# Kernel optimization log

Measured on AMD Instinct MI355X. Metric: run time of the kernel, lower is better.

## Reference

```python
import jax, jax.numpy as jnp
import numpy as np

H, D, K = 8, 512, 64
EPS = 1e-12


def _l2norm(x):
    # F.normalize(p=2, dim=-1): x / max(||x||_2, eps)
    n = jnp.sqrt(jnp.sum(x * x, axis=-1, keepdims=True))
    return x / jnp.maximum(n, EPS)


def setup_inputs() -> dict:
    key = jax.random.key(0)
    ks = jax.random.split(key, 8)
    S, B = 1024, 16
    scale = 1.0 / np.sqrt(D)
    return {
        "query": jax.random.normal(ks[0], (S, B, D), dtype=jnp.float32),
        "key": jax.random.normal(ks[1], (S, B, D), dtype=jnp.float32),
        "value": jax.random.normal(ks[2], (S, B, D), dtype=jnp.float32),
        # stacked per-head projection weights, torch Linear convention [out,in]
        "WQ": jax.random.uniform(ks[3], (H, K, D), jnp.float32, -scale, scale),
        "WK": jax.random.uniform(ks[4], (H, K, D), jnp.float32, -scale, scale),
        "WV": jax.random.uniform(ks[5], (H, K, D), jnp.float32, -scale, scale),
        "Wout": jax.random.uniform(ks[6], (D, H * K), jnp.float32,
                                   -1.0 / np.sqrt(H * K), 1.0 / np.sqrt(H * K)),
    }


def reference(query, key, value, WQ, WK, WV, Wout):
    temp = K ** 0.5
    # project all heads at once: [S,B,D] x [H,K,D] -> [B,H,S,K]
    wq = _l2norm(jnp.einsum("sbd,hkd->bhsk", query, WQ))
    wk = _l2norm(jnp.einsum("sbd,hkd->bhsk", key, WK))
    wv = _l2norm(jnp.einsum("sbd,hkd->bhsk", value, WV))
    # cosine-similarity attention scores [B,H,Sq,Sk]
    scores = jnp.einsum("bhsk,bhtk->bhst", wq, wk) / temp
    aff = jax.nn.softmax(scores, axis=-1)
    out = jnp.einsum("bhst,bhtk->bhsk", aff, wv)  # [B,H,S,K]
    # concat heads -> [S,B,H*K] (matches torch per-head concat on last dim)
    Sq, B = query.shape[0], query.shape[1]
    concat = out.transpose(2, 0, 1, 3).reshape(Sq, B, H * K)
    return concat @ Wout.T  # [S,B,D]
```

## Files before the change

kernel.cpp:

```cpp
#include <hip/hip_runtime.h>
#include <cstdint>
#include <cstddef>

typedef unsigned int u32;
typedef unsigned short u16;
typedef __attribute__((ext_vector_type(8))) short short8;
typedef __attribute__((ext_vector_type(4))) float f32x4;

#define S_LEN 1024
#define BATCH 16
#define NHEAD 8
#define DMODEL 512
#define KHD 64
#define NROW (S_LEN * BATCH)

__device__ __forceinline__ u16 f2bf(float f) {
    u32 u = __float_as_uint(f);
    return (u16)((u + 0x7fffu + ((u >> 16) & 1u)) >> 16);
}

__device__ __forceinline__ void gl_lds16(const void* g, void* l) {
    __builtin_amdgcn_global_load_lds(
        (const __attribute__((address_space(1))) void*)(uintptr_t)g,
        (__attribute__((address_space(3))) void*)(uintptr_t)l, 16, 0, 0);
}

__global__ __launch_bounds__(256) void wcvt_kernel(
    const float* __restrict__ WQ, const float* __restrict__ WK,
    const float* __restrict__ WV, const float* __restrict__ Wo,
    u16* __restrict__ dst)
{
    const int m = blockIdx.y;
    const float* __restrict__ src = (m == 0) ? WQ : (m == 1) ? WK : (m == 2) ? WV : Wo;
    const int idx = (blockIdx.x * 256 + threadIdx.x) * 4;
    const float4 v = *(const float4*)(src + idx);
    u16 r[4];
    r[0] = f2bf(v.x); r[1] = f2bf(v.y); r[2] = f2bf(v.z); r[3] = f2bf(v.w);
    *(uint2*)(dst + (size_t)m * DMODEL * DMODEL + idx) = *(uint2*)r;
}

__global__ __launch_bounds__(256) void xcvt_kernel(
    const float* __restrict__ s0, const float* __restrict__ s1,
    u16* __restrict__ dst)
{
    const float* __restrict__ src = (blockIdx.y == 0) ? s0 : s1;
    u16* d = dst + (size_t)blockIdx.y * NROW * DMODEL;
    const int idx = (blockIdx.x * 256 + threadIdx.x) * 4;
    const float4 v = *(const float4*)(src + idx);
    u16 r[4];
    r[0] = f2bf(v.x); r[1] = f2bf(v.y); r[2] = f2bf(v.z); r[3] = f2bf(v.w);
    *(uint2*)(d + idx) = *(uint2*)r;
}

template<int M>
__global__ __launch_bounds__(256) void gemm_kernel(
    const u16* __restrict__ Abf,
    const u16* __restrict__ Wb,
    u16* __restrict__ outN,
    float* __restrict__ outP)
{
    __shared__ __align__(16) u16 Alds[128 * 64];
    __shared__ __align__(16) u16 Blds[128 * 64];

    const int tid  = threadIdx.x;
    const int wave = tid >> 6;
    const int lane = tid & 63;
    const int m16  = lane & 15;
    const int quad = lane >> 4;
    const int wm   = wave >> 1;
    const int wn   = wave & 1;
    const int n0   = blockIdx.y * 128;
    const int row0 = blockIdx.x * 128;
    const int z    = (M == 1) ? blockIdx.z : 0;
    const int bb   = (M == 2) ? blockIdx.z : 0;

    const u16* __restrict__ A = Abf + (size_t)z * NROW * DMODEL + (size_t)bb * DMODEL;
    const size_t astr = (M == 2) ? (size_t)BATCH * DMODEL : (size_t)DMODEL;
    const u16* __restrict__ B = Wb + ((M == 1) ? (size_t)z * DMODEL * DMODEL : 0);

    f32x4 acc[4][4] = {};

    const int brow   = lane >> 3;
    const int bchunk = (lane & 7) ^ brow;

    for (int kt = 0; kt < DMODEL; kt += 64) {
        __syncthreads();
        {
            const u16* ap = A + (size_t)(row0 + wave * 32 + brow) * astr + kt + bchunk * 8;
            const u16* bp = B + (size_t)(n0 + wave * 32 + brow) * DMODEL + kt + bchunk * 8;
            u16* la = &Alds[(wave * 32) * 64];
            u16* lb = &Blds[(wave * 32) * 64];
#pragma unroll
            for (int j = 0; j < 4; j++) {
                gl_lds16(ap + (size_t)j * 8 * astr,   la + j * 8 * 64);
                gl_lds16(bp + (size_t)j * 8 * DMODEL, lb + j * 8 * 64);
            }
        }
        __syncthreads();

#pragma unroll
        for (int half = 0; half < 2; half++) {
            short8 af[4], bfr[4];
#pragma unroll
            for (int mt = 0; mt < 4; mt++)
                af[mt] = *(const short8*)&Alds[(wm * 64 + mt * 16 + m16) * 64 +
                                               (((half << 2) + quad) ^ (m16 & 7)) * 8];
#pragma unroll
            for (int nt = 0; nt < 4; nt++)
                bfr[nt] = *(const short8*)&Blds[(wn * 64 + nt * 16 + m16) * 64 +
                                                (((half << 2) + quad) ^ (m16 & 7)) * 8];
#pragma unroll
            for (int mt = 0; mt < 4; mt++)
#pragma unroll
                for (int nt = 0; nt < 4; nt++)
                    acc[mt][nt] = __builtin_amdgcn_mfma_f32_16x16x32_bf16(af[mt], bfr[nt], acc[mt][nt], 0, 0, 0);
        }
    }

    if (M == 1) {
        const int h = (n0 >> 6) + wn;
        u16* outZ = outN + (size_t)z * BATCH * NHEAD * S_LEN * KHD;
#pragma unroll
        for (int mt = 0; mt < 4; mt++) {
#pragma unroll
            for (int r = 0; r < 4; r++) {
                float ss = 0.0f;
#pragma unroll
                for (int nt = 0; nt < 4; nt++) ss += acc[mt][nt][r] * acc[mt][nt][r];
                ss += __shfl_xor(ss, 1);
                ss += __shfl_xor(ss, 2);
                ss += __shfl_xor(ss, 4);
                ss += __shfl_xor(ss, 8);
                const float sc = 1.0f / fmaxf(sqrtf(ss), 1e-12f);
                const int i = row0 + wm * 64 + mt * 16 + quad * 4 + r;
                const int s = i >> 4, b = i & 15;
                u16* op = outZ + (((size_t)b * NHEAD + h) * S_LEN + s) * KHD;
#pragma unroll
                for (int nt = 0; nt < 4; nt++)
                    op[nt * 16 + m16] = f2bf(acc[mt][nt][r] * sc);
            }
        }
    } else if (M == 2) {
        const int h = (n0 >> 6) + wn;
#pragma unroll
        for (int mt = 0; mt < 4; mt++) {
            float scl[4];
#pragma unroll
            for (int r = 0; r < 4; r++) {
                float ss = 0.0f;
#pragma unroll
                for (int nt = 0; nt < 4; nt++) ss += acc[mt][nt][r] * acc[mt][nt][r];
                ss += __shfl_xor(ss, 1);
                ss += __shfl_xor(ss, 2);
                ss += __shfl_xor(ss, 4);
                ss += __shfl_xor(ss, 8);
                scl[r] = 1.0f / fmaxf(sqrtf(ss), 1e-12f);
            }
            const int sbase = row0 + wm * 64 + mt * 16 + quad * 4;
#pragma unroll
            for (int nt = 0; nt < 4; nt++) {
                const int vcol = nt * 16 + m16;
                uint2 pk;
                pk.x = (u32)f2bf(acc[mt][nt][0] * scl[0]) |
                       ((u32)f2bf(acc[mt][nt][1] * scl[1]) << 16);
                pk.y = (u32)f2bf(acc[mt][nt][2] * scl[2]) |
                       ((u32)f2bf(acc[mt][nt][3] * scl[3]) << 16);
                u16* dp = outN + (((size_t)bb * NHEAD + h) * KHD + vcol) * S_LEN + sbase;
                *(uint2*)dp = pk;
            }
        }
    } else {
#pragma unroll
        for (int mt = 0; mt < 4; mt++) {
#pragma unroll
            for (int r = 0; r < 4; r++) {
                const int i = row0 + wm * 64 + mt * 16 + quad * 4 + r;
                float* op = outP + (size_t)i * DMODEL + n0 + wn * 64;
#pragma unroll
                for (int nt = 0; nt < 4; nt++)
                    op[nt * 16 + m16] = acc[mt][nt][r];
            }
        }
    }
}

__global__ __launch_bounds__(256, 4) void attn_kernel(
    const u16* __restrict__ wq, const u16* __restrict__ wk, const u16* __restrict__ wvT,
    u16* __restrict__ Xc)
{
    __shared__ __align__(16) u16 Klds[2][64 * 64];
    __shared__ __align__(16) u16 Vlds[2][64 * 64];
    __shared__ __align__(16) u16 Plds[4][2][16 * 32];

    const int tid  = threadIdx.x;
    const int wave = tid >> 6;
    const int lane = tid & 63;
    const int m16  = lane & 15;
    const int quad = lane >> 4;
    const int bh   = blockIdx.x;
    const int qt   = blockIdx.y;

    const u16* Qb = wq  + (size_t)bh * S_LEN * KHD;
    const u16* Kb = wk  + (size_t)bh * S_LEN * KHD;
    const u16* Vb = wvT + (size_t)bh * KHD * S_LEN;

    const int qr0 = qt * 128 + wave * 32 + m16;
    short8 qf[2][2];
    qf[0][0] = *(const short8*)(Qb + (size_t)qr0 * KHD + quad * 8);
    qf[0][1] = *(const short8*)(Qb + (size_t)qr0 * KHD + 32 + quad * 8);
    qf[1][0] = *(const short8*)(Qb + (size_t)(qr0 + 16) * KHD + quad * 8);
    qf[1][1] = *(const short8*)(Qb + (size_t)(qr0 + 16) * KHD + 32 + quad * 8);

    short8 ones;
#pragma unroll
    for (int j = 0; j < 8; j++) ones[j] = (short)0x3F80;

    f32x4 o[2][4] = {};
    f32x4 ls[2]   = {};
    const float C1 = 0.125f, C2 = 0.0078125f;

    const int srow   = lane >> 3;
    const int schunk = (lane & 7) ^ srow;
    const int r0     = wave * 8 + srow;
    const int pswz   = (m16 >> 1) & 3;

    gl_lds16(Kb + (size_t)r0 * KHD + schunk * 8,               &Klds[0][(wave * 8) * 64]);
    gl_lds16(Kb + (size_t)(r0 + 32) * KHD + schunk * 8,        &Klds[0][(wave * 8 + 32) * 64]);
    gl_lds16(Vb + (size_t)r0 * S_LEN + schunk * 8,             &Vlds[0][(wave * 8) * 64]);
    gl_lds16(Vb + (size_t)(r0 + 32) * S_LEN + schunk * 8,      &Vlds[0][(wave * 8 + 32) * 64]);
    __syncthreads();

    for (int it = 0; it < S_LEN / 64; it++) {
        const int cur = it & 1;

        if (it + 1 < S_LEN / 64) {
            const int nxt = cur ^ 1;
            const int kt0 = (it + 1) * 64;
            gl_lds16(Kb + (size_t)(kt0 + r0) * KHD + schunk * 8,        &Klds[nxt][(wave * 8) * 64]);
            gl_lds16(Kb + (size_t)(kt0 + r0 + 32) * KHD + schunk * 8,   &Klds[nxt][(wave * 8 + 32) * 64]);
            gl_lds16(Vb + (size_t)r0 * S_LEN + kt0 + schunk * 8,        &Vlds[nxt][(wave * 8) * 64]);
            gl_lds16(Vb + (size_t)(r0 + 32) * S_LEN + kt0 + schunk * 8, &Vlds[nxt][(wave * 8 + 32) * 64]);
        }

#pragma unroll
        for (int cc = 0; cc < 2; cc++) {
#pragma unroll
            for (int mm = 0; mm < 2; mm++) {
                const int mt = cc * 2 + mm;
                const short8 kf0 = *(const short8*)&Klds[cur][(mt * 16 + m16) * 64 + (quad ^ (m16 & 7)) * 8];
                const short8 kf1 = *(const short8*)&Klds[cur][(mt * 16 + m16) * 64 + ((4 + quad) ^ (m16 & 7)) * 8];
#pragma unroll
                for (int qb = 0; qb < 2; qb++) {
                    f32x4 s = {};
                    s = __builtin_amdgcn_mfma_f32_16x16x32_bf16(kf0, qf[qb][0], s, 0, 0, 0);
                    s = __builtin_amdgcn_mfma_f32_16x16x32_bf16(kf1, qf[qb][1], s, 0, 0, 0);
                    u32 up[4];
#pragma unroll
                    for (int r = 0; r < 4; r++) {
                        const float y = s[r];
                        const float p = fmaf(fmaf(C2, y, C1), y, 1.0f);
                        up[r] = __float_as_uint(p);
                    }
                    uint2 pk;
                    pk.x = __builtin_amdgcn_perm(up[1], up[0], 0x07060302u);
                    pk.y = __builtin_amdgcn_perm(up[3], up[2], 0x07060302u);
                    *(uint2*)((char*)&Plds[wave][qb][0] + m16 * 64 +
                              ((((mm << 1) + (quad >> 1)) ^ pswz) << 4) + ((quad & 1) << 3)) = pk;
                }
            }

            short8 vfr[4];
#pragma unroll
            for (int vt = 0; vt < 4; vt++)
                vfr[vt] = *(const short8*)&Vlds[cur][(vt * 16 + m16) * 64 +
                                                     (((cc << 2) + quad) ^ (m16 & 7)) * 8];
            __builtin_amdgcn_s_setprio(1);
#pragma unroll
            for (int qb = 0; qb < 2; qb++) {
                const short8 pb = *(const short8*)((const char*)&Plds[wave][qb][0] + m16 * 64 +
                                                   ((quad ^ pswz) << 4));
                ls[qb] = __builtin_amdgcn_mfma_f32_16x16x32_bf16(ones, pb, ls[qb], 0, 0, 0);
#pragma unroll
                for (int vt = 0; vt < 4; vt++)
                    o[qb][vt] = __builtin_amdgcn_mfma_f32_16x16x32_bf16(vfr[vt], pb, o[qb][vt], 0, 0, 0);
            }
            __builtin_amdgcn_s_setprio(0);
        }

        __syncthreads();
    }

    const int b = bh >> 3, h = bh & 7;
#pragma unroll
    for (int qb = 0; qb < 2; qb++) {
        const float inv = 1.0f / ls[qb][0];
        const int qrow = qr0 + qb * 16;
        u16* cp = Xc + ((size_t)qrow * BATCH + b) * (NHEAD * KHD) + h * KHD;
#pragma unroll
        for (int vt = 0; vt < 4; vt++) {
            uint2 pk;
            pk.x = (u32)f2bf(o[qb][vt][0] * inv) | ((u32)f2bf(o[qb][vt][1] * inv) << 16);
            pk.y = (u32)f2bf(o[qb][vt][2] * inv) | ((u32)f2bf(o[qb][vt][3] * inv) << 16);
            *(uint2*)(cp + vt * 16 + quad * 4) = pk;
        }
    }
}

extern "C" void kernel_launch(void* const* d_in, const int* in_sizes, int n_in,
                              void* d_out, int out_size, void* d_ws, size_t ws_size,
                              hipStream_t stream) {
    const float* q    = (const float*)d_in[0];
    const float* k    = (const float*)d_in[1];
    const float* v    = (const float*)d_in[2];
    const float* WQ   = (const float*)d_in[3];
    const float* WK   = (const float*)d_in[4];
    const float* WV   = (const float*)d_in[5];
    const float* Wout = (const float*)d_in[6];
    float* out = (float*)d_out;
    u16*  Xbf = (u16*)d_out;

    const size_t per = (size_t)BATCH * NHEAD * S_LEN * KHD;
    u16* wsQKV = (u16*)d_ws;
    u16* wsW   = wsQKV + 3 * per;

    wcvt_kernel<<<dim3(256, 4), 256, 0, stream>>>(WQ, WK, WV, Wout, wsW);

    xcvt_kernel<<<dim3(NROW * DMODEL / 1024, 2), 256, 0, stream>>>(q, k, Xbf);

    gemm_kernel<1><<<dim3(NROW / 128, DMODEL / 128, 2), 256, 0, stream>>>(
        Xbf, wsW, wsQKV, nullptr);

    xcvt_kernel<<<dim3(NROW * DMODEL / 1024, 1), 256, 0, stream>>>(v, v, Xbf);

    gemm_kernel<2><<<dim3(S_LEN / 128, DMODEL / 128, BATCH), 256, 0, stream>>>(
        Xbf, wsW + (size_t)2 * DMODEL * DMODEL, wsQKV + 2 * per, nullptr);

    attn_kernel<<<dim3(BATCH * NHEAD, S_LEN / 128), 256, 0, stream>>>(
        wsQKV, wsQKV + per, wsQKV + 2 * per, Xbf);

    hipMemcpyAsync(wsQKV, Xbf, (size_t)NROW * DMODEL * sizeof(u16),
                   hipMemcpyDeviceToDevice, stream);

    gemm_kernel<0><<<dim3(NROW / 128, DMODEL / 128, 1), 256, 0, stream>>>(
        wsQKV, wsW + (size_t)3 * DMODEL * DMODEL, nullptr, out);
}
```

Before: 260.1 us.

## Write attention output head-major in place and gather it in output GEMM

The attention kernel now writes its bf16 output per (batch, head) into the Q workspace region instead of the interleaved concat layout. This removes the device-to-device memcpy that used to sit before the output projection. The output GEMM's A-tile load now gathers from the head-major layout by mapping each row and column to batch, seq, head and k indices. Separately, each attention block now handles 256 query rows (4 q-subtiles per wave) with launch bounds relaxed to 2, which raises K/V reuse per LDS load but halves the grid and increases register pressure.

```diff
diff --git a/kernel.cpp b/kernel.cpp
--- a/kernel.cpp
+++ b/kernel.cpp
@@ -86,14 +86,28 @@
     for (int kt = 0; kt < DMODEL; kt += 64) {
         __syncthreads();
         {
-            const u16* ap = A + (size_t)(row0 + wave * 32 + brow) * astr + kt + bchunk * 8;
-            const u16* bp = B + (size_t)(n0 + wave * 32 + brow) * DMODEL + kt + bchunk * 8;
             u16* la = &Alds[(wave * 32) * 64];
             u16* lb = &Blds[(wave * 32) * 64];
-#pragma unroll
-            for (int j = 0; j < 4; j++) {
-                gl_lds16(ap + (size_t)j * 8 * astr,   la + j * 8 * 64);
-                gl_lds16(bp + (size_t)j * 8 * DMODEL, lb + j * 8 * 64);
+            const u16* bp = B + (size_t)(n0 + wave * 32 + brow) * DMODEL + kt + bchunk * 8;
+            if (M == 0) {
+                const int colc = kt + bchunk * 8;
+                const int hh   = colc >> 6;
+                const int kk   = colc & 63;
+#pragma unroll
+                for (int j = 0; j < 4; j++) {
+                    const int i  = row0 + wave * 32 + brow + j * 8;
+                    const int ss = i >> 4, bx = i & 15;
+                    gl_lds16(Abf + (((size_t)(bx * NHEAD + hh) * S_LEN + ss) * KHD + kk),
+                             la + j * 8 * 64);
+                    gl_lds16(bp + (size_t)j * 8 * DMODEL, lb + j * 8 * 64);
+                }
+            } else {
+                const u16* ap = A + (size_t)(row0 + wave * 32 + brow) * astr + kt + bchunk * 8;
+#pragma unroll
+                for (int j = 0; j < 4; j++) {
+                    gl_lds16(ap + (size_t)j * 8 * astr,   la + j * 8 * 64);
+                    gl_lds16(bp + (size_t)j * 8 * DMODEL, lb + j * 8 * 64);
+                }
             }
         }
         __syncthreads();
@@ -184,13 +198,13 @@
     }
 }
 
-__global__ __launch_bounds__(256, 4) void attn_kernel(
+__global__ __launch_bounds__(256, 2) void attn_kernel(
     const u16* __restrict__ wq, const u16* __restrict__ wk, const u16* __restrict__ wvT,
-    u16* __restrict__ Xc)
+    u16* __restrict__ Xout)
 {
     __shared__ __align__(16) u16 Klds[2][64 * 64];
     __shared__ __align__(16) u16 Vlds[2][64 * 64];
-    __shared__ __align__(16) u16 Plds[4][2][16 * 32];
+    __shared__ __align__(16) u16 Plds[4][4][16 * 32];
 
     const int tid  = threadIdx.x;
     const int wave = tid >> 6;
@@ -204,19 +218,20 @@
     const u16* Kb = wk  + (size_t)bh * S_LEN * KHD;
     const u16* Vb = wvT + (size_t)bh * KHD * S_LEN;
 
-    const int qr0 = qt * 128 + wave * 32 + m16;
-    short8 qf[2][2];
-    qf[0][0] = *(const short8*)(Qb + (size_t)qr0 * KHD + quad * 8);
-    qf[0][1] = *(const short8*)(Qb + (size_t)qr0 * KHD + 32 + quad * 8);
-    qf[1][0] = *(const short8*)(Qb + (size_t)(qr0 + 16) * KHD + quad * 8);
-    qf[1][1] = *(const short8*)(Qb + (size_t)(qr0 + 16) * KHD + 32 + quad * 8);
+    const int qr0 = qt * 256 + wave * 64;
+    short8 qf[4][2];
+#pragma unroll
+    for (int qb = 0; qb < 4; qb++) {
+        qf[qb][0] = *(const short8*)(Qb + (size_t)(qr0 + qb * 16 + m16) * KHD + quad * 8);
+        qf[qb][1] = *(const short8*)(Qb + (size_t)(qr0 + qb * 16 + m16) * KHD + 32 + quad * 8);
+    }
 
     short8 ones;
 #pragma unroll
     for (int j = 0; j < 8; j++) ones[j] = (short)0x3F80;
 
-    f32x4 o[2][4] = {};
-    f32x4 ls[2]   = {};
+    f32x4 o[4][4] = {};
+    f32x4 ls[4]   = {};
     const float C1 = 0.125f, C2 = 0.0078125f;
 
     const int srow   = lane >> 3;
@@ -250,7 +265,7 @@
                 const short8 kf0 = *(const short8*)&Klds[cur][(mt * 16 + m16) * 64 + (quad ^ (m16 & 7)) * 8];
                 const short8 kf1 = *(const short8*)&Klds[cur][(mt * 16 + m16) * 64 + ((4 + quad) ^ (m16 & 7)) * 8];
 #pragma unroll
-                for (int qb = 0; qb < 2; qb++) {
+                for (int qb = 0; qb < 4; qb++) {
                     f32x4 s = {};
                     s = __builtin_amdgcn_mfma_f32_16x16x32_bf16(kf0, qf[qb][0], s, 0, 0, 0);
                     s = __builtin_amdgcn_mfma_f32_16x16x32_bf16(kf1, qf[qb][1], s, 0, 0, 0);
@@ -276,7 +291,7 @@
                                                      (((cc << 2) + quad) ^ (m16 & 7)) * 8];
             __builtin_amdgcn_s_setprio(1);
 #pragma unroll
-            for (int qb = 0; qb < 2; qb++) {
+            for (int qb = 0; qb < 4; qb++) {
                 const short8 pb = *(const short8*)((const char*)&Plds[wave][qb][0] + m16 * 64 +
                                                    ((quad ^ pswz) << 4));
                 ls[qb] = __builtin_amdgcn_mfma_f32_16x16x32_bf16(ones, pb, ls[qb], 0, 0, 0);
@@ -290,12 +305,12 @@
         __syncthreads();
     }
 
-    const int b = bh >> 3, h = bh & 7;
-#pragma unroll
-    for (int qb = 0; qb < 2; qb++) {
+    u16* outB = Xout + (size_t)bh * S_LEN * KHD;
+#pragma unroll
+    for (int qb = 0; qb < 4; qb++) {
         const float inv = 1.0f / ls[qb][0];
-        const int qrow = qr0 + qb * 16;
-        u16* cp = Xc + ((size_t)qrow * BATCH + b) * (NHEAD * KHD) + h * KHD;
+        const int qrow = qr0 + qb * 16 + m16;
+        u16* cp = outB + (size_t)qrow * KHD;
 #pragma unroll
         for (int vt = 0; vt < 4; vt++) {
             uint2 pk;
@@ -335,11 +350,8 @@
     gemm_kernel<2><<<dim3(S_LEN / 128, DMODEL / 128, BATCH), 256, 0, stream>>>(
         Xbf, wsW + (size_t)2 * DMODEL * DMODEL, wsQKV + 2 * per, nullptr);
 
-    attn_kernel<<<dim3(BATCH * NHEAD, S_LEN / 128), 256, 0, stream>>>(
-        wsQKV, wsQKV + per, wsQKV + 2 * per, Xbf);
-
-    hipMemcpyAsync(wsQKV, Xbf, (size_t)NROW * DMODEL * sizeof(u16),
-                   hipMemcpyDeviceToDevice, stream);
+    attn_kernel<<<dim3(BATCH * NHEAD, S_LEN / 256), 256, 0, stream>>>(
+        wsQKV, wsQKV + per, wsQKV + 2 * per, wsQKV);
 
     gemm_kernel<0><<<dim3(NROW / 128, DMODEL / 128, 1), 256, 0, stream>>>(
         wsQKV, wsW + (size_t)3 * DMODEL * DMODEL, nullptr, out);
```

Measured after the change: 250.8 us. 1.04x faster.
